# Kernel optimization log

Measured on AMD Instinct MI355X. Metric: run time of the kernel, lower is better.

Reference implementation:

```python
import jax, jax.numpy as jnp
import numpy as np

# Static feature-pyramid shapes (stride 8/16/32 of a 512x512 image)
SPATIAL_SHAPES = ((64, 64), (32, 32), (16, 16))
SEQ = sum(h * w for h, w in SPATIAL_SHAPES)  # 5376
B, D, NH, NL, NP = 4, 256, 8, 3, 4
DH = D // NH  # 32


def _reference_points():
    # normalized pixel centers per level, valid_ratios == 1
    refs = []
    for (h, w) in SPATIAL_SHAPES:
        ry = (jnp.arange(h, dtype=jnp.float32) + 0.5) / h
        rx = (jnp.arange(w, dtype=jnp.float32) + 0.5) / w
        yy, xx = jnp.meshgrid(ry, rx, indexing='ij')
        refs.append(jnp.stack([xx.reshape(-1), yy.reshape(-1)], -1))  # [h*w, 2]
    ref = jnp.concatenate(refs, 0)  # [S, 2]
    return jnp.broadcast_to(ref[None, :, None, :], (B, SEQ, NL, 2))


def setup_inputs() -> dict:
    key = jax.random.key(0)
    ks = jax.random.split(key, 8)
    s = 0.02
    return {
        'hidden_states': jax.random.normal(ks[0], (B, SEQ, D), jnp.float32),
        'position_embeddings': jax.random.normal(ks[1], (B, SEQ, D), jnp.float32),
        'reference_points': _reference_points(),
        'Wv': jax.random.normal(ks[2], (D, D), jnp.float32) * s,
        'bv': jnp.zeros((D,), jnp.float32),
        'Wo': jax.random.normal(ks[3], (D, NH * NL * NP * 2), jnp.float32) * s,
        'bo': jax.random.normal(ks[4], (NH * NL * NP * 2,), jnp.float32) * 0.1,
        'Wa': jax.random.normal(ks[5], (D, NH * NL * NP), jnp.float32) * s,
        'ba': jnp.zeros((NH * NL * NP,), jnp.float32),
        'Wout': jax.random.normal(ks[6], (D, D), jnp.float32) * s,
        'bout': jnp.zeros((D,), jnp.float32),
    }


def _bilinear_sample(img, gx, gy):
    # img: [N, C, H, W]; gx, gy: [N, Q, P] in [-1, 1]
    # grid_sample(mode='bilinear', padding_mode='zeros', align_corners=False)
    N, C, H, W = img.shape
    x = (gx + 1.0) * (W * 0.5) - 0.5
    y = (gy + 1.0) * (H * 0.5) - 0.5
    x0 = jnp.floor(x)
    y0 = jnp.floor(y)
    wx, wy = x - x0, y - y0
    flat = img.reshape(N, C, H * W)
    out = jnp.zeros((N, C) + gx.shape[1:], img.dtype)
    for xi, wxi in ((x0, 1.0 - wx), (x0 + 1.0, wx)):
        for yi, wyi in ((y0, 1.0 - wy), (y0 + 1.0, wy)):
            valid = (xi >= 0) & (xi < W) & (yi >= 0) & (yi < H)
            xc = jnp.clip(xi, 0, W - 1).astype(jnp.int32)
            yc = jnp.clip(yi, 0, H - 1).astype(jnp.int32)
            idx = (yc * W + xc).reshape(N, 1, -1)  # [N,1,Q*P]
            v = jnp.take_along_axis(flat, idx, axis=2).reshape(N, C, *gx.shape[1:])
            out = out + v * (wxi * wyi * valid.astype(img.dtype))[:, None]
    return out  # [N, C, Q, P]


def reference(hidden_states, position_embeddings, reference_points,
              Wv, bv, Wo, bo, Wa, ba, Wout, bout):
    hs = hidden_states + position_embeddings  # queries carry pos embed
    value = hidden_states @ Wv + bv           # value from raw encoder states
    value = value.reshape(B, SEQ, NH, DH)

    off = (hs @ Wo + bo).reshape(B, SEQ, NH, NL, NP, 2)
    attn = jax.nn.softmax((hs @ Wa + ba).reshape(B, SEQ, NH, NL * NP), -1)
    attn = attn.reshape(B, SEQ, NH, NL, NP)

    # offset normalizer: [W_l, H_l] per level
    norm = jnp.array([[w, h] for (h, w) in SPATIAL_SHAPES], jnp.float32)
    loc = reference_points[:, :, None, :, None, :] + off / norm[None, None, None, :, None, :]
    grid = 2.0 * loc - 1.0  # [B, Q, H, L, P, 2]

    sampled = []
    start = 0
    for lvl, (h, w) in enumerate(SPATIAL_SHAPES):
        v_l = value[:, start:start + h * w]  # [B, h*w, H, d]
        start += h * w
        v_l = v_l.transpose(0, 2, 3, 1).reshape(B * NH, DH, h, w)
        g_l = grid[:, :, :, lvl].transpose(0, 2, 1, 3, 4).reshape(B * NH, SEQ, NP, 2)
        sampled.append(_bilinear_sample(v_l, g_l[..., 0], g_l[..., 1]))  # [B*H,d,Q,P]
    sampled = jnp.stack(sampled, -2).reshape(B * NH, DH, SEQ, NL * NP)

    aw = attn.transpose(0, 2, 1, 3, 4).reshape(B * NH, 1, SEQ, NL * NP)
    out = (sampled * aw).sum(-1)                   # [B*H, d, Q]
    out = out.reshape(B, NH * DH, SEQ).transpose(0, 2, 1)  # [B, Q, D]
    out = out @ Wout + bout
    return out, attn
```

## Files before the change

### kernel.cpp

```cpp
#include <hip/hip_runtime.h>
#include <hip/hip_bf16.h>
#include <math.h>

#define BB 4
#define SEQ 5376
#define DD 256
#define NH 8
#define NL 3
#define NP 4
#define DH 32
#define MTOT (BB * SEQ)

typedef __attribute__((ext_vector_type(8))) short bf16x8;
typedef __attribute__((ext_vector_type(4))) float f32x4;
typedef __attribute__((ext_vector_type(2))) float f32x2;

#define GLD_LDS16(src, dst) __builtin_amdgcn_global_load_lds( \
    (const __attribute__((address_space(1))) void*)(src),     \
    (__attribute__((address_space(3))) void*)(dst), 16, 0, 0)

__device__ __forceinline__ ushort f2b(float f) {
    __hip_bfloat16 h = __float2bfloat16(f);
    return *reinterpret_cast<ushort*>(&h);
}

__global__ __launch_bounds__(256) void prep_all(
    const float* __restrict__ hidden, const float* __restrict__ pos,
    const float* __restrict__ Wv, const float* __restrict__ Wo,
    const float* __restrict__ Wa, const float* __restrict__ Wout,
    const float* __restrict__ bo, const float* __restrict__ ba,
    ushort4* __restrict__ hb, ushort4* __restrict__ hsb,
    ushort* __restrict__ Wt, float* __restrict__ bcomb, int n4) {
    int bid = blockIdx.x;
    int tid = threadIdx.x;
    if (bid <= 800) {
        if (bid == 800) {
            for (int i = tid; i < 288; i += 256)
                bcomb[i] = (i < 192) ? bo[i] : ba[i - 192];
            return;
        }
        int row = bid;
        const float* src;
        int N, n;
        if (row < 256)      { src = Wv;   N = 256; n = row; }
        else if (row < 448) { src = Wo;   N = 192; n = row - 256; }
        else if (row < 544) { src = Wa;   N = 96;  n = row - 448; }
        else                { src = Wout; N = 256; n = row - 544; }
        float v = src[(size_t)tid * N + n];
        Wt[(size_t)row * 256 + tid] = f2b(v);
        return;
    }
    const float4* h4 = (const float4*)hidden;
    const float4* p4 = (const float4*)pos;
    int i = (bid - 801) * 256 + tid;
    int stride = (gridDim.x - 801) * 256;
    for (; i < n4; i += stride) {
        float4 a = h4[i], b = p4[i];
        ushort4 ua, us;
        ua.x = f2b(a.x); ua.y = f2b(a.y); ua.z = f2b(a.z); ua.w = f2b(a.w);
        us.x = f2b(a.x + b.x); us.y = f2b(a.y + b.y);
        us.z = f2b(a.z + b.z); us.w = f2b(a.w + b.w);
        hb[i] = ua;
        hsb[i] = us;
    }
}

__global__ __launch_bounds__(256) void gemm_dual(
    const ushort* __restrict__ hb, const ushort* __restrict__ hsb,
    const ushort* __restrict__ Wv_t, const ushort* __restrict__ Wcomb_t,
    const float* __restrict__ bv, const float* __restrict__ bcomb,
    ushort* __restrict__ value_bf, float* __restrict__ comb) {
    const int K = 256, BK = 64;
    __shared__ ushort As[128 * 64];
    __shared__ ushort Bs[128 * 64];

    int b = blockIdx.x;
    const ushort* A;
    const ushort* W;
    const float* bias;
    int bn, bm, N;
    bool obf;
    if (b < 336) {
        A = hb;  W = Wv_t;    bias = bv;    N = 256; obf = true;
        bn = (b & 1) * 128;   bm = (b >> 1) * 128;
    } else {
        int bb = b - 336;
        A = hsb; W = Wcomb_t; bias = bcomb; N = 288; obf = false;
        bn = (bb % 3) * 128;  bm = (bb / 3) * 128;
    }

    int tid = threadIdx.x;
    int lane = tid & 63;
    int wid = tid >> 6;
    int wr = wid >> 1, wc = wid & 1;
    int lr = lane & 15;
    int kg = lane >> 4;

    f32x4 acc[4][4] = {};

    for (int k0 = 0; k0 < K; k0 += BK) {
        #pragma unroll
        for (int c = 0; c < 4; c++) {
            int e = tid + 256 * c;
            int row = e >> 3;
            int ch = e & 7;
            int gch = ch ^ (row & 7);
            GLD_LDS16(A + (size_t)(bm + row) * K + k0 + 8 * gch, &As[e * 8]);
            GLD_LDS16(W + (size_t)(bn + row) * K + k0 + 8 * gch, &Bs[e * 8]);
        }
        __syncthreads();
        #pragma unroll
        for (int ks = 0; ks < 2; ks++) {
            bf16x8 af[4], bfr[4];
            #pragma unroll
            for (int mf = 0; mf < 4; mf++) {
                int R = wr * 64 + mf * 16 + lr;
                int sc = (ks * 4 + kg) ^ (R & 7);
                af[mf] = *(bf16x8*)&As[R * 64 + sc * 8];
            }
            #pragma unroll
            for (int nf = 0; nf < 4; nf++) {
                int R = wc * 64 + nf * 16 + lr;
                int sc = (ks * 4 + kg) ^ (R & 7);
                bfr[nf] = *(bf16x8*)&Bs[R * 64 + sc * 8];
            }
            #pragma unroll
            for (int mf = 0; mf < 4; mf++)
                #pragma unroll
                for (int nf = 0; nf < 4; nf++)
                    acc[mf][nf] = __builtin_amdgcn_mfma_f32_16x16x32_bf16(
                        af[mf], bfr[nf], acc[mf][nf], 0, 0, 0);
        }
        __syncthreads();
    }

    #pragma unroll
    for (int nf = 0; nf < 4; nf++) {
        int gc = bn + wc * 64 + nf * 16 + lr;
        if (gc >= N) continue;
        float bvv = bias[gc];
        #pragma unroll
        for (int mf = 0; mf < 4; mf++) {
            int gr0 = bm + wr * 64 + mf * 16 + kg * 4;
            #pragma unroll
            for (int r = 0; r < 4; r++) {
                float v = acc[mf][nf][r] + bvv;
                if (obf)
                    value_bf[(size_t)(gr0 + r) * 256 + gc] = f2b(v);
                else
                    comb[(size_t)(gr0 + r) * 288 + gc] = v;
            }
        }
    }
}

__global__ __launch_bounds__(256) void gemm_out(
    const ushort* __restrict__ A, const ushort* __restrict__ Wt,
    const float* __restrict__ bias, float* __restrict__ C) {
    const int K = 256, BK = 64;
    __shared__ ushort As[128 * 64];
    __shared__ ushort Bs[64 * 64];
    int bm = blockIdx.y * 128;
    int bn = blockIdx.x * 64;
    int tid = threadIdx.x;
    int lane = tid & 63;
    int wid = tid >> 6;
    int wr = wid >> 1, wc = wid & 1;
    int lr = lane & 15;
    int kg = lane >> 4;

    f32x4 acc[4][2] = {};

    for (int k0 = 0; k0 < K; k0 += BK) {
        #pragma unroll
        for (int c = 0; c < 4; c++) {
            int e = tid + 256 * c;
            int row = e >> 3;
            int ch = e & 7;
            int gch = ch ^ (row & 7);
            GLD_LDS16(A + (size_t)(bm + row) * K + k0 + 8 * gch, &As[e * 8]);
        }
        #pragma unroll
        for (int c = 0; c < 2; c++) {
            int e = tid + 256 * c;
            int row = e >> 3;
            int ch = e & 7;
            int gch = ch ^ (row & 7);
            GLD_LDS16(Wt + (size_t)(bn + row) * K + k0 + 8 * gch, &Bs[e * 8]);
        }
        __syncthreads();
        #pragma unroll
        for (int ks = 0; ks < 2; ks++) {
            bf16x8 af[4], bfr[2];
            #pragma unroll
            for (int mf = 0; mf < 4; mf++) {
                int R = wr * 64 + mf * 16 + lr;
                int sc = (ks * 4 + kg) ^ (R & 7);
                af[mf] = *(bf16x8*)&As[R * 64 + sc * 8];
            }
            #pragma unroll
            for (int nf = 0; nf < 2; nf++) {
                int R = wc * 32 + nf * 16 + lr;
                int sc = (ks * 4 + kg) ^ (R & 7);
                bfr[nf] = *(bf16x8*)&Bs[R * 64 + sc * 8];
            }
            #pragma unroll
            for (int mf = 0; mf < 4; mf++)
                #pragma unroll
                for (int nf = 0; nf < 2; nf++)
                    acc[mf][nf] = __builtin_amdgcn_mfma_f32_16x16x32_bf16(
                        af[mf], bfr[nf], acc[mf][nf], 0, 0, 0);
        }
        __syncthreads();
    }

    #pragma unroll
    for (int nf = 0; nf < 2; nf++) {
        int gc = bn + wc * 32 + nf * 16 + lr;
        float bvv = bias[gc];
        #pragma unroll
        for (int mf = 0; mf < 4; mf++) {
            int gr0 = bm + wr * 64 + mf * 16 + kg * 4;
            #pragma unroll
            for (int r = 0; r < 4; r++) {
                C[(size_t)(gr0 + r) * 256 + gc] = acc[mf][nf][r] + bvv;
            }
        }
    }
}

__device__ __forceinline__ void fma8p(f32x2 acc[4], float wt, uint4 u) {
    f32x2 w2 = {wt, wt};
    uint p0 = u.x, p1 = u.y, p2 = u.z, p3 = u.w;
    f32x2 v0, v1, v2, v3;
    v0[0] = __uint_as_float(p0 << 16); v0[1] = __uint_as_float(p0 & 0xffff0000u);
    v1[0] = __uint_as_float(p1 << 16); v1[1] = __uint_as_float(p1 & 0xffff0000u);
    v2[0] = __uint_as_float(p2 << 16); v2[1] = __uint_as_float(p2 & 0xffff0000u);
    v3[0] = __uint_as_float(p3 << 16); v3[1] = __uint_as_float(p3 & 0xffff0000u);
    acc[0] = __builtin_elementwise_fma(v0, w2, acc[0]);
    acc[1] = __builtin_elementwise_fma(v1, w2, acc[1]);
    acc[2] = __builtin_elementwise_fma(v2, w2, acc[2]);
    acc[3] = __builtin_elementwise_fma(v3, w2, acc[3]);
}

__global__ __launch_bounds__(128) void msda_sample_v11(
    const ushort* __restrict__ value, const float* __restrict__ comb,
    const float* __restrict__ refp, float* __restrict__ attn_out,
    ushort* __restrict__ out) {
    __shared__ int4   s_idx[4][8][13];
    __shared__ float4 s_w[4][8][13];
    int tid = threadIdx.x;
    int bq0 = blockIdx.x * 4;

    #pragma unroll
    for (int it = 0; it < 4; it++) {
        int t = tid + it * 128;
        int lp = t & 15;
        int qh = t >> 4;
        int q = qh >> 3, h = qh & 7;
        int bq = bq0 + q;
        bool active = lp < 12;
        const float* crow = comb + (size_t)bq * 288;
        float logit = active ? crow[192 + h * 12 + lp] : -INFINITY;
        float m = logit;
        m = fmaxf(m, __shfl_xor(m, 1, 16));
        m = fmaxf(m, __shfl_xor(m, 2, 16));
        m = fmaxf(m, __shfl_xor(m, 4, 16));
        m = fmaxf(m, __shfl_xor(m, 8, 16));
        float e = active ? expf(logit - m) : 0.f;
        float s = e;
        s += __shfl_xor(s, 1, 16);
        s += __shfl_xor(s, 2, 16);
        s += __shfl_xor(s, 4, 16);
        s += __shfl_xor(s, 8, 16);
        float aw = e / s;
        if (active) {
            attn_out[(size_t)bq * 96 + h * 12 + lp] = aw;
            int l = lp >> 2;
            int b = bq / SEQ;
            int Wl = 64 >> l;
            float fW = (float)Wl;
            float rx = refp[(size_t)bq * 6 + 2 * l];
            float ry = refp[(size_t)bq * 6 + 2 * l + 1];
            float ox = crow[h * 24 + lp * 2];
            float oy = crow[h * 24 + lp * 2 + 1];
            float x = rx * fW + ox - 0.5f;
            float y = ry * fW + oy - 0.5f;
            float x0f = floorf(x), y0f = floorf(y);
            float wx = x - x0f, wy = y - y0f;
            int x0 = (int)x0f, y0 = (int)y0f;
            int x1 = x0 + 1, y1 = y0 + 1;
            float vx0 = (x0 >= 0 && x0 < Wl) ? 1.f : 0.f;
            float vx1 = (x1 >= 0 && x1 < Wl) ? 1.f : 0.f;
            float vy0 = (y0 >= 0 && y0 < Wl) ? 1.f : 0.f;
            float vy1 = (y1 >= 0 && y1 < Wl) ? 1.f : 0.f;
            int xc0 = min(max(x0, 0), Wl - 1);
            int xc1 = min(max(x1, 0), Wl - 1);
            int yc0 = min(max(y0, 0), Wl - 1);
            int yc1 = min(max(y1, 0), Wl - 1);
            int st = (l == 0) ? 0 : ((l == 1) ? 4096 : 5120);
            int rowbase = b * SEQ + st;
            s_idx[q][h][lp] = make_int4((rowbase + yc0 * Wl + xc0) << 8,
                                        (rowbase + yc0 * Wl + xc1) << 8,
                                        (rowbase + yc1 * Wl + xc0) << 8,
                                        (rowbase + yc1 * Wl + xc1) << 8);
            s_w[q][h][lp] = make_float4(aw * (1.f - wx) * (1.f - wy) * vx0 * vy0,
                                        aw * wx * (1.f - wy) * vx1 * vy0,
                                        aw * (1.f - wx) * wy * vx0 * vy1,
                                        aw * wx * wy * vx1 * vy1);
        }
    }
    __syncthreads();

    int wave = tid >> 6, lane = tid & 63;
    int q2 = lane >> 5;
    int lane5 = lane & 31;
    int h = lane5 >> 2, d8 = lane5 & 3;
    int q = wave * 2 + q2;
    int bq = bq0 + q;
    int ch0 = h * 32 + d8 * 8;
    const ushort* vb = value + ch0;

    f32x2 acc[4] = {{0.f, 0.f}, {0.f, 0.f}, {0.f, 0.f}, {0.f, 0.f}};
    #pragma unroll
    for (int lp = 0; lp < 12; lp++) {
        int4 ii = s_idx[q][h][lp];
        float4 ww = s_w[q][h][lp];
        uint4 u0 = *(const uint4*)(vb + ii.x);
        uint4 u1 = *(const uint4*)(vb + ii.y);
        uint4 u2 = *(const uint4*)(vb + ii.z);
        uint4 u3 = *(const uint4*)(vb + ii.w);
        fma8p(acc, ww.x, u0);
        fma8p(acc, ww.y, u1);
        fma8p(acc, ww.z, u2);
        fma8p(acc, ww.w, u3);
    }

    bf16x8 o;
    o[0] = (short)f2b(acc[0][0]); o[1] = (short)f2b(acc[0][1]);
    o[2] = (short)f2b(acc[1][0]); o[3] = (short)f2b(acc[1][1]);
    o[4] = (short)f2b(acc[2][0]); o[5] = (short)f2b(acc[2][1]);
    o[6] = (short)f2b(acc[3][0]); o[7] = (short)f2b(acc[3][1]);
    *(bf16x8*)(out + (size_t)bq * 256 + ch0) = o;
}

extern "C" void kernel_launch(void* const* d_in, const int* in_sizes, int n_in,
                              void* d_out, int out_size, void* d_ws, size_t ws_size,
                              hipStream_t stream) {
    const float* hidden = (const float*)d_in[0];
    const float* pos    = (const float*)d_in[1];
    const float* refp   = (const float*)d_in[2];
    const float* Wv     = (const float*)d_in[3];
    const float* bv     = (const float*)d_in[4];
    const float* Wo     = (const float*)d_in[5];
    const float* bo     = (const float*)d_in[6];
    const float* Wa     = (const float*)d_in[7];
    const float* ba     = (const float*)d_in[8];
    const float* Wout   = (const float*)d_in[9];
    const float* bout   = (const float*)d_in[10];

    float* out      = (float*)d_out;
    float* attn_out = out + (size_t)BB * SEQ * DD;

    const size_t BSD = (size_t)BB * SEQ * DD;
    char* w = (char*)d_ws;
    ushort* value_bf = (ushort*)w;  w += BSD * 2;
    float*  comb     = (float*)w;   w += (size_t)MTOT * 288 * 4;
    ushort* sampb    = (ushort*)w;  w += BSD * 2;
    ushort* hb       = (ushort*)w;  w += BSD * 2;
    ushort* hsb      = (ushort*)w;  w += BSD * 2;
    ushort* Wt       = (ushort*)w;  w += (size_t)800 * 256 * 2;
    float*  bcomb    = (float*)w;

    {
        int n4 = (int)(BSD / 4);
        prep_all<<<801 + 2048, 256, 0, stream>>>(hidden, pos, Wv, Wo, Wa, Wout,
                                                 bo, ba, (ushort4*)hb, (ushort4*)hsb,
                                                 Wt, bcomb, n4);
    }

    const ushort* Wv_t    = Wt;
    const ushort* Wcomb_t = Wt + (size_t)256 * 256;
    const ushort* Wout_t  = Wt + (size_t)544 * 256;

    gemm_dual<<<840, 256, 0, stream>>>(hb, hsb, Wv_t, Wcomb_t, bv, bcomb,
                                       value_bf, comb);

    msda_sample_v11<<<MTOT / 4, 128, 0, stream>>>(value_bf, comb, refp,
                                                  attn_out, sampb);

    {
        dim3 grid(DD / 64, MTOT / 128);
        gemm_out<<<grid, 256, 0, stream>>>(sampb, Wout_t, bout, out);
    }
}
```

Measured before the change: 80.49 us.

## Store value head-major and fetch adjacent x-pixels as one contiguous 128-byte span

The value GEMM now writes its bf16 output head-major ([head][row][32]), so the two horizontally adjacent corner pixels of a bilinear sample sit next to each other in memory. The sampler clamps the left x index to Wl-2 and remaps the x weights to match. Each sample then needs two row fetches instead of four scattered ones, with lanes split across the pixel pair and their partial sums combined by a shuffle. Blocks shrink from 4 to 2 queries, which doubles the grid. The change lowers the number of gather transactions, but half the lanes finish without storing and the weight-remapping logic adds branches.

```diff
diff --git a/kernel.cpp b/kernel.cpp
--- a/kernel.cpp
+++ b/kernel.cpp
@@ -145,10 +145,13 @@
             #pragma unroll
             for (int r = 0; r < 4; r++) {
                 float v = acc[mf][nf][r] + bvv;
-                if (obf)
-                    value_bf[(size_t)(gr0 + r) * 256 + gc] = f2b(v);
-                else
+                if (obf) {
+                    int hh = gc >> 5, cc = gc & 31;
+                    value_bf[(size_t)hh * ((size_t)MTOT * 32)
+                             + (size_t)(gr0 + r) * 32 + cc] = f2b(v);
+                } else {
                     comb[(size_t)(gr0 + r) * 288 + gc] = v;
+                }
             }
         }
     }
@@ -231,29 +234,28 @@
 
 __device__ __forceinline__ void fma8p(f32x2 acc[4], float wt, uint4 u) {
     f32x2 w2 = {wt, wt};
-    uint p0 = u.x, p1 = u.y, p2 = u.z, p3 = u.w;
     f32x2 v0, v1, v2, v3;
-    v0[0] = __uint_as_float(p0 << 16); v0[1] = __uint_as_float(p0 & 0xffff0000u);
-    v1[0] = __uint_as_float(p1 << 16); v1[1] = __uint_as_float(p1 & 0xffff0000u);
-    v2[0] = __uint_as_float(p2 << 16); v2[1] = __uint_as_float(p2 & 0xffff0000u);
-    v3[0] = __uint_as_float(p3 << 16); v3[1] = __uint_as_float(p3 & 0xffff0000u);
+    v0[0] = __uint_as_float(u.x << 16); v0[1] = __uint_as_float(u.x & 0xffff0000u);
+    v1[0] = __uint_as_float(u.y << 16); v1[1] = __uint_as_float(u.y & 0xffff0000u);
+    v2[0] = __uint_as_float(u.z << 16); v2[1] = __uint_as_float(u.z & 0xffff0000u);
+    v3[0] = __uint_as_float(u.w << 16); v3[1] = __uint_as_float(u.w & 0xffff0000u);
     acc[0] = __builtin_elementwise_fma(v0, w2, acc[0]);
     acc[1] = __builtin_elementwise_fma(v1, w2, acc[1]);
     acc[2] = __builtin_elementwise_fma(v2, w2, acc[2]);
     acc[3] = __builtin_elementwise_fma(v3, w2, acc[3]);
 }
 
-__global__ __launch_bounds__(128) void msda_sample_v11(
+__global__ __launch_bounds__(128) void msda_sample_v12(
     const ushort* __restrict__ value, const float* __restrict__ comb,
     const float* __restrict__ refp, float* __restrict__ attn_out,
     ushort* __restrict__ out) {
-    __shared__ int4   s_idx[4][8][13];
-    __shared__ float4 s_w[4][8][13];
+    __shared__ int2   s_idx[2][8][13];
+    __shared__ float4 s_w[2][8][13];
     int tid = threadIdx.x;
-    int bq0 = blockIdx.x * 4;
+    int bq0 = blockIdx.x * 2;
 
     #pragma unroll
-    for (int it = 0; it < 4; it++) {
+    for (int it = 0; it < 2; it++) {
         int t = tid + it * 128;
         int lp = t & 15;
         int qh = t >> 4;
@@ -294,54 +296,63 @@
             float vx1 = (x1 >= 0 && x1 < Wl) ? 1.f : 0.f;
             float vy0 = (y0 >= 0 && y0 < Wl) ? 1.f : 0.f;
             float vy1 = (y1 >= 0 && y1 < Wl) ? 1.f : 0.f;
-            int xc0 = min(max(x0, 0), Wl - 1);
-            int xc1 = min(max(x1, 0), Wl - 1);
             int yc0 = min(max(y0, 0), Wl - 1);
             int yc1 = min(max(y1, 0), Wl - 1);
+            int px = min(max(x0, 0), Wl - 2);
+            float wxl = (1.f - wx) * vx0;
+            float wxh = wx * vx1;
+            float wA, wB;
+            if (px == x0)      { wA = wxl; wB = wxh; }
+            else if (px == x1) { wA = wxh; wB = 0.f; }
+            else               { wA = 0.f; wB = wxl; }
+            float wy0v = aw * (1.f - wy) * vy0;
+            float wy1v = aw * wy * vy1;
             int st = (l == 0) ? 0 : ((l == 1) ? 4096 : 5120);
             int rowbase = b * SEQ + st;
-            s_idx[q][h][lp] = make_int4((rowbase + yc0 * Wl + xc0) << 8,
-                                        (rowbase + yc0 * Wl + xc1) << 8,
-                                        (rowbase + yc1 * Wl + xc0) << 8,
-                                        (rowbase + yc1 * Wl + xc1) << 8);
-            s_w[q][h][lp] = make_float4(aw * (1.f - wx) * (1.f - wy) * vx0 * vy0,
-                                        aw * wx * (1.f - wy) * vx1 * vy0,
-                                        aw * (1.f - wx) * wy * vx0 * vy1,
-                                        aw * wx * wy * vx1 * vy1);
+            s_idx[q][h][lp] = make_int2((rowbase + yc0 * Wl + px) * 32,
+                                        (rowbase + yc1 * Wl + px) * 32);
+            s_w[q][h][lp] = make_float4(wA * wy0v, wB * wy0v,
+                                        wA * wy1v, wB * wy1v);
         }
     }
     __syncthreads();
 
     int wave = tid >> 6, lane = tid & 63;
-    int q2 = lane >> 5;
-    int lane5 = lane & 31;
-    int h = lane5 >> 2, d8 = lane5 & 3;
-    int q = wave * 2 + q2;
+    int q = wave;
     int bq = bq0 + q;
-    int ch0 = h * 32 + d8 * 8;
-    const ushort* vb = value + ch0;
+    int h = lane >> 3;
+    int d8 = lane & 7;
+    int part = d8 >> 2;
+    int c4 = d8 & 3;
+    const ushort* vb = value + (size_t)h * ((size_t)MTOT * 32)
+                       + part * 32 + c4 * 8;
 
     f32x2 acc[4] = {{0.f, 0.f}, {0.f, 0.f}, {0.f, 0.f}, {0.f, 0.f}};
     #pragma unroll
     for (int lp = 0; lp < 12; lp++) {
-        int4 ii = s_idx[q][h][lp];
+        int2 ii = s_idx[q][h][lp];
         float4 ww = s_w[q][h][lp];
+        float w0 = part ? ww.y : ww.x;
+        float w1 = part ? ww.w : ww.z;
         uint4 u0 = *(const uint4*)(vb + ii.x);
         uint4 u1 = *(const uint4*)(vb + ii.y);
-        uint4 u2 = *(const uint4*)(vb + ii.z);
-        uint4 u3 = *(const uint4*)(vb + ii.w);
-        fma8p(acc, ww.x, u0);
-        fma8p(acc, ww.y, u1);
-        fma8p(acc, ww.z, u2);
-        fma8p(acc, ww.w, u3);
-    }
-
-    bf16x8 o;
-    o[0] = (short)f2b(acc[0][0]); o[1] = (short)f2b(acc[0][1]);
-    o[2] = (short)f2b(acc[1][0]); o[3] = (short)f2b(acc[1][1]);
-    o[4] = (short)f2b(acc[2][0]); o[5] = (short)f2b(acc[2][1]);
-    o[6] = (short)f2b(acc[3][0]); o[7] = (short)f2b(acc[3][1]);
-    *(bf16x8*)(out + (size_t)bq * 256 + ch0) = o;
+        fma8p(acc, w0, u0);
+        fma8p(acc, w1, u1);
+    }
+
+    #pragma unroll
+    for (int i = 0; i < 4; i++) {
+        acc[i][0] += __shfl_xor(acc[i][0], 4);
+        acc[i][1] += __shfl_xor(acc[i][1], 4);
+    }
+    if (part == 0) {
+        bf16x8 o;
+        o[0] = (short)f2b(acc[0][0]); o[1] = (short)f2b(acc[0][1]);
+        o[2] = (short)f2b(acc[1][0]); o[3] = (short)f2b(acc[1][1]);
+        o[4] = (short)f2b(acc[2][0]); o[5] = (short)f2b(acc[2][1]);
+        o[6] = (short)f2b(acc[3][0]); o[7] = (short)f2b(acc[3][1]);
+        *(bf16x8*)(out + (size_t)bq * 256 + h * 32 + c4 * 8) = o;
+    }
 }
 
 extern "C" void kernel_launch(void* const* d_in, const int* in_sizes, int n_in,
@@ -386,7 +397,7 @@
     gemm_dual<<<840, 256, 0, stream>>>(hb, hsb, Wv_t, Wcomb_t, bv, bcomb,
                                        value_bf, comb);
 
-    msda_sample_v11<<<MTOT / 4, 128, 0, stream>>>(value_bf, comb, refp,
+    msda_sample_v12<<<MTOT / 2, 128, 0, stream>>>(value_bf, comb, refp,
                                                   attn_out, sampb);
 
     {
```

Result: faster. 78.21 us (median of 2 runs) (-2.8%).
